# Kernel optimization log

Measured on AMD Instinct MI355X. Metric: run time of the kernel, lower is better.

The kernel has to match this reference:

```python
import jax, jax.numpy as jnp
import numpy as np

B, S, H = 32, 512, 768
VOCAB, MAX_POS, TYPE_VOCAB = 30522, 512, 2
N_COLS, MAX_HLEN = 32, 16
EPS = 1e-12


def setup_inputs() -> dict:
    key = jax.random.key(0)
    ks = jax.random.split(key, 16)
    input_ids = jax.random.randint(ks[0], (B, S), 0, VOCAB)
    header_ids = jax.random.randint(ks[1], (B, N_COLS, MAX_HLEN), 0, VOCAB)
    token_type_ids = jax.random.randint(ks[2], (B, S), 0, TYPE_VOCAB)
    match_type_ids = jax.random.randint(ks[3], (B, S), 0, 11)
    type_idx = jax.random.randint(ks[4], (B, S), 0, 6)
    # distinct scatter positions per batch row (the original dict keys ki are unique)
    col_pos = jnp.sort(jnp.argsort(jax.random.uniform(ks[5], (B, S)), axis=1)[:, :N_COLS], axis=1)
    col_idx = jax.random.randint(ks[6], (B, N_COLS), 0, N_COLS)
    header_len = jax.random.randint(ks[7], (B, N_COLS), 0, MAX_HLEN + 1)  # 0 -> skip
    word_emb = jax.random.normal(ks[8], (VOCAB, H), dtype=jnp.float32) * 0.02
    pos_emb = jax.random.normal(ks[9], (MAX_POS, H), dtype=jnp.float32) * 0.02
    tok_type_emb = jax.random.normal(ks[10], (TYPE_VOCAB, H), dtype=jnp.float32) * 0.02
    match_emb = jax.random.normal(ks[11], (11, H), dtype=jnp.float32) * 0.02
    type_emb = jax.random.normal(ks[12], (6, H), dtype=jnp.float32) * 0.02
    ln_w = jnp.ones((H,), dtype=jnp.float32)
    ln_b = jnp.zeros((H,), dtype=jnp.float32)
    return {"input_ids": input_ids, "header_ids": header_ids,
            "token_type_ids": token_type_ids, "match_type_ids": match_type_ids,
            "type_idx": type_idx, "col_pos": col_pos, "col_idx": col_idx,
            "header_len": header_len, "word_emb": word_emb, "pos_emb": pos_emb,
            "tok_type_emb": tok_type_emb, "match_emb": match_emb,
            "type_emb": type_emb, "ln_w": ln_w, "ln_b": ln_b}


def reference(input_ids, header_ids, token_type_ids, match_type_ids, type_idx,
              col_pos, col_idx, header_len, word_emb, pos_emb, tok_type_emb,
              match_emb, type_emb, ln_w, ln_b):
    b, s = input_ids.shape
    words = word_emb[input_ids]                    # [B,S,H]
    header = word_emb[header_ids]                  # [B,C,L,H]
    L = header_ids.shape[2]
    # variable-length mean pool over header tokens
    mask = (jnp.arange(L)[None, None, :] < header_len[:, :, None]).astype(words.dtype)
    denom = jnp.maximum(header_len, 1).astype(words.dtype)[..., None]
    pooled = jnp.einsum('bclh,bcl->bch', header, mask) / denom   # [B,C,H]
    # scatter pooled column embeddings into word embeddings at col_pos (skip len==0)
    b_idx = jnp.arange(b)[:, None]
    sel = pooled[b_idx, col_idx]                   # [B,C,H]
    valid = (header_len[b_idx, col_idx] > 0)[..., None]
    cur = words[b_idx, col_pos]
    words = words.at[b_idx, col_pos].set(jnp.where(valid, sel, cur))
    emb = (words
           + pos_emb[jnp.arange(s)][None, :, :]
           + tok_type_emb[token_type_ids]
           + match_emb[match_type_ids]
           + type_emb[type_idx])
    # TF-style LayerNorm (eps inside sqrt)
    u = emb.mean(-1, keepdims=True)
    var = jnp.square(emb - u).mean(-1, keepdims=True)
    x = (emb - u) / jnp.sqrt(var + EPS)
    return ln_w * x + ln_b
```

## Files before the change

### kernel.cpp

```cpp
#include <hip/hip_runtime.h>

#define B_ 32
#define S_ 512
#define H_ 768
#define C_ 32
#define L_ 16

__global__ __launch_bounds__(256) void bert_emb_kernel(
    const int* __restrict__ input_ids,
    const int* __restrict__ header_ids,
    const int* __restrict__ token_type_ids,
    const int* __restrict__ match_type_ids,
    const int* __restrict__ type_idx,
    const int* __restrict__ col_pos,
    const int* __restrict__ col_idx,
    const int* __restrict__ header_len,
    const float* __restrict__ word_emb,
    const float* __restrict__ pos_emb,
    const float* __restrict__ tok_type_emb,
    const float* __restrict__ match_emb,
    const float* __restrict__ type_emb,
    const float* __restrict__ ln_w,
    const float* __restrict__ ln_b,
    float* __restrict__ out)
{
    const int tok  = blockIdx.x * 4 + (threadIdx.x >> 6);
    const int lane = threadIdx.x & 63;
    const int b    = tok >> 9;
    const int s    = tok & (S_ - 1);

    const int cq = lane & 31;
    const int cp = col_pos[(b << 5) + cq];
    unsigned long long m = __ballot(cp == s) & 0xffffffffULL;
    int use_pool = 0, ci = 0, hlen = 0;
    if (m) {
        const int cm = __ffsll((unsigned long long)m) - 1;
        ci   = col_idx[(b << 5) + cm];
        hlen = header_len[(b << 5) + ci];
        use_pool = (hlen > 0);
    }

    const int h = lane << 2;
    float a0x, a0y, a0z, a0w, a1x, a1y, a1z, a1w, a2x, a2y, a2z, a2w;

    if (use_pool) {
        a0x=a0y=a0z=a0w=a1x=a1y=a1z=a1w=a2x=a2y=a2z=a2w=0.f;
        const int* hid = header_ids + ((b << 5) + ci) * L_;
        for (int l = 0; l < hlen; ++l) {
            const float* r = word_emb + (size_t)hid[l] * H_ + h;
            float4 v0 = *reinterpret_cast<const float4*>(r);
            float4 v1 = *reinterpret_cast<const float4*>(r + 256);
            float4 v2 = *reinterpret_cast<const float4*>(r + 512);
            a0x+=v0.x; a0y+=v0.y; a0z+=v0.z; a0w+=v0.w;
            a1x+=v1.x; a1y+=v1.y; a1z+=v1.z; a1w+=v1.w;
            a2x+=v2.x; a2y+=v2.y; a2z+=v2.z; a2w+=v2.w;
        }
        const float inv = 1.0f / (float)hlen;
        a0x*=inv; a0y*=inv; a0z*=inv; a0w*=inv;
        a1x*=inv; a1y*=inv; a1z*=inv; a1w*=inv;
        a2x*=inv; a2y*=inv; a2z*=inv; a2w*=inv;
    } else {
        const float* r = word_emb + (size_t)input_ids[tok] * H_ + h;
        float4 v0 = *reinterpret_cast<const float4*>(r);
        float4 v1 = *reinterpret_cast<const float4*>(r + 256);
        float4 v2 = *reinterpret_cast<const float4*>(r + 512);
        a0x=v0.x; a0y=v0.y; a0z=v0.z; a0w=v0.w;
        a1x=v1.x; a1y=v1.y; a1z=v1.z; a1w=v1.w;
        a2x=v2.x; a2y=v2.y; a2z=v2.z; a2w=v2.w;
    }

    {
        const float* r = pos_emb + s * H_ + h;
        float4 v0 = *reinterpret_cast<const float4*>(r);
        float4 v1 = *reinterpret_cast<const float4*>(r + 256);
        float4 v2 = *reinterpret_cast<const float4*>(r + 512);
        a0x+=v0.x; a0y+=v0.y; a0z+=v0.z; a0w+=v0.w;
        a1x+=v1.x; a1y+=v1.y; a1z+=v1.z; a1w+=v1.w;
        a2x+=v2.x; a2y+=v2.y; a2z+=v2.z; a2w+=v2.w;
    }
    {
        const float* r = tok_type_emb + token_type_ids[tok] * H_ + h;
        float4 v0 = *reinterpret_cast<const float4*>(r);
        float4 v1 = *reinterpret_cast<const float4*>(r + 256);
        float4 v2 = *reinterpret_cast<const float4*>(r + 512);
        a0x+=v0.x; a0y+=v0.y; a0z+=v0.z; a0w+=v0.w;
        a1x+=v1.x; a1y+=v1.y; a1z+=v1.z; a1w+=v1.w;
        a2x+=v2.x; a2y+=v2.y; a2z+=v2.z; a2w+=v2.w;
    }
    {
        const float* r = match_emb + match_type_ids[tok] * H_ + h;
        float4 v0 = *reinterpret_cast<const float4*>(r);
        float4 v1 = *reinterpret_cast<const float4*>(r + 256);
        float4 v2 = *reinterpret_cast<const float4*>(r + 512);
        a0x+=v0.x; a0y+=v0.y; a0z+=v0.z; a0w+=v0.w;
        a1x+=v1.x; a1y+=v1.y; a1z+=v1.z; a1w+=v1.w;
        a2x+=v2.x; a2y+=v2.y; a2z+=v2.z; a2w+=v2.w;
    }
    {
        const float* r = type_emb + type_idx[tok] * H_ + h;
        float4 v0 = *reinterpret_cast<const float4*>(r);
        float4 v1 = *reinterpret_cast<const float4*>(r + 256);
        float4 v2 = *reinterpret_cast<const float4*>(r + 512);
        a0x+=v0.x; a0y+=v0.y; a0z+=v0.z; a0w+=v0.w;
        a1x+=v1.x; a1y+=v1.y; a1z+=v1.z; a1w+=v1.w;
        a2x+=v2.x; a2y+=v2.y; a2z+=v2.z; a2w+=v2.w;
    }

    float s1 = a0x+a0y+a0z+a0w + a1x+a1y+a1z+a1w + a2x+a2y+a2z+a2w;
    float s2 = a0x*a0x+a0y*a0y+a0z*a0z+a0w*a0w
             + a1x*a1x+a1y*a1y+a1z*a1z+a1w*a1w
             + a2x*a2x+a2y*a2y+a2z*a2z+a2w*a2w;
    #pragma unroll
    for (int off = 32; off > 0; off >>= 1) {
        s1 += __shfl_xor(s1, off);
        s2 += __shfl_xor(s2, off);
    }
    const float mean = s1 * (1.0f / H_);
    float var = s2 * (1.0f / H_) - mean * mean;
    var = fmaxf(var, 0.0f);
    const float rstd = rsqrtf(var + 1e-12f);

    const float* wp = ln_w + h;
    const float* bp = ln_b + h;
    float* op = out + (size_t)tok * H_ + h;
    {
        float4 w = *reinterpret_cast<const float4*>(wp);
        float4 c = *reinterpret_cast<const float4*>(bp);
        float4 o;
        o.x=(a0x-mean)*rstd*w.x+c.x; o.y=(a0y-mean)*rstd*w.y+c.y;
        o.z=(a0z-mean)*rstd*w.z+c.z; o.w=(a0w-mean)*rstd*w.w+c.w;
        *reinterpret_cast<float4*>(op) = o;
    }
    {
        float4 w = *reinterpret_cast<const float4*>(wp + 256);
        float4 c = *reinterpret_cast<const float4*>(bp + 256);
        float4 o;
        o.x=(a1x-mean)*rstd*w.x+c.x; o.y=(a1y-mean)*rstd*w.y+c.y;
        o.z=(a1z-mean)*rstd*w.z+c.z; o.w=(a1w-mean)*rstd*w.w+c.w;
        *reinterpret_cast<float4*>(op + 256) = o;
    }
    {
        float4 w = *reinterpret_cast<const float4*>(wp + 512);
        float4 c = *reinterpret_cast<const float4*>(bp + 512);
        float4 o;
        o.x=(a2x-mean)*rstd*w.x+c.x; o.y=(a2y-mean)*rstd*w.y+c.y;
        o.z=(a2z-mean)*rstd*w.z+c.z; o.w=(a2w-mean)*rstd*w.w+c.w;
        *reinterpret_cast<float4*>(op + 512) = o;
    }
}

extern "C" void kernel_launch(void* const* d_in, const int* in_sizes, int n_in,
                              void* d_out, int out_size, void* d_ws, size_t ws_size,
                              hipStream_t stream) {
    const int* input_ids      = (const int*)d_in[0];
    const int* header_ids     = (const int*)d_in[1];
    const int* token_type_ids = (const int*)d_in[2];
    const int* match_type_ids = (const int*)d_in[3];
    const int* type_idx       = (const int*)d_in[4];
    const int* col_pos        = (const int*)d_in[5];
    const int* col_idx        = (const int*)d_in[6];
    const int* header_len     = (const int*)d_in[7];
    const float* word_emb     = (const float*)d_in[8];
    const float* pos_emb      = (const float*)d_in[9];
    const float* tok_type_emb = (const float*)d_in[10];
    const float* match_emb    = (const float*)d_in[11];
    const float* type_emb     = (const float*)d_in[12];
    const float* ln_w         = (const float*)d_in[13];
    const float* ln_b         = (const float*)d_in[14];
    float* out = (float*)d_out;

    bert_emb_kernel<<<(B_ * S_) / 4, 256, 0, stream>>>(
        input_ids, header_ids, token_type_ids, match_type_ids, type_idx,
        col_pos, col_idx, header_len, word_emb, pos_emb, tok_type_emb,
        match_emb, type_emb, ln_w, ln_b, out);
}
```

Baseline: 191.2 us.

## Precompute header mean-pooling in a separate kernel and use nontemporal output stores

A new pre-kernel computes the mean-pooled header embeddings for every column into workspace memory. The main kernel then reads one pooled row for scatter positions, so the variable-length gather loop no longer sits inside the per-token kernel and wave divergence goes away. Output writes now use nontemporal stores. The cost is an extra kernel launch, a workspace round trip, and pooling every column even when it is never selected.

```diff
diff --git a/kernel.cpp b/kernel.cpp
--- a/kernel.cpp
+++ b/kernel.cpp
@@ -5,10 +5,43 @@
 #define H_ 768
 #define C_ 32
 #define L_ 16
+#define VOCAB_ 30522
+
+typedef float f4 __attribute__((ext_vector_type(4)));
+
+__device__ __forceinline__ f4 ld4(const float* p) {
+    return *reinterpret_cast<const f4*>(p);
+}
+
+__global__ __launch_bounds__(256) void pool_kernel(
+    const int* __restrict__ header_ids,
+    const int* __restrict__ header_len,
+    const float* __restrict__ word_emb,
+    float* __restrict__ pooled)
+{
+    const int wi   = blockIdx.x * 4 + (threadIdx.x >> 6);
+    const int lane = threadIdx.x & 63;
+    const int hlen = header_len[wi];
+    if (hlen <= 0) return;
+
+    const int h = lane << 2;
+    const int* hid = header_ids + wi * L_;
+    f4 a0 = {0,0,0,0}, a1 = {0,0,0,0}, a2 = {0,0,0,0};
+    for (int l = 0; l < hlen; ++l) {
+        const float* r = word_emb + (size_t)hid[l] * H_ + h;
+        a0 += ld4(r);
+        a1 += ld4(r + 256);
+        a2 += ld4(r + 512);
+    }
+    const float inv = 1.0f / (float)hlen;
+    float* o = pooled + (size_t)wi * H_ + h;
+    *reinterpret_cast<f4*>(o)       = a0 * inv;
+    *reinterpret_cast<f4*>(o + 256) = a1 * inv;
+    *reinterpret_cast<f4*>(o + 512) = a2 * inv;
+}
 
 __global__ __launch_bounds__(256) void bert_emb_kernel(
     const int* __restrict__ input_ids,
-    const int* __restrict__ header_ids,
     const int* __restrict__ token_type_ids,
     const int* __restrict__ match_type_ids,
     const int* __restrict__ type_idx,
@@ -22,6 +55,7 @@
     const float* __restrict__ type_emb,
     const float* __restrict__ ln_w,
     const float* __restrict__ ln_b,
+    const float* __restrict__ pooled,
     float* __restrict__ out)
 {
     const int tok  = blockIdx.x * 4 + (threadIdx.x >> 6);
@@ -29,123 +63,69 @@
     const int b    = tok >> 9;
     const int s    = tok & (S_ - 1);
 
-    const int cq = lane & 31;
-    const int cp = col_pos[(b << 5) + cq];
+    const int cp = col_pos[(b << 5) + (lane & 31)];
     unsigned long long m = __ballot(cp == s) & 0xffffffffULL;
-    int use_pool = 0, ci = 0, hlen = 0;
+    const float* wrow;
     if (m) {
-        const int cm = __ffsll((unsigned long long)m) - 1;
-        ci   = col_idx[(b << 5) + cm];
-        hlen = header_len[(b << 5) + ci];
-        use_pool = (hlen > 0);
+        const int cm = __ffsll(m) - 1;
+        const int ci = col_idx[(b << 5) + cm];
+        if (header_len[(b << 5) + ci] > 0)
+            wrow = pooled + (size_t)((b << 5) + ci) * H_;
+        else
+            wrow = word_emb + (size_t)input_ids[tok] * H_;
+    } else {
+        wrow = word_emb + (size_t)input_ids[tok] * H_;
     }
 
     const int h = lane << 2;
-    float a0x, a0y, a0z, a0w, a1x, a1y, a1z, a1w, a2x, a2y, a2z, a2w;
-
-    if (use_pool) {
-        a0x=a0y=a0z=a0w=a1x=a1y=a1z=a1w=a2x=a2y=a2z=a2w=0.f;
-        const int* hid = header_ids + ((b << 5) + ci) * L_;
-        for (int l = 0; l < hlen; ++l) {
-            const float* r = word_emb + (size_t)hid[l] * H_ + h;
-            float4 v0 = *reinterpret_cast<const float4*>(r);
-            float4 v1 = *reinterpret_cast<const float4*>(r + 256);
-            float4 v2 = *reinterpret_cast<const float4*>(r + 512);
-            a0x+=v0.x; a0y+=v0.y; a0z+=v0.z; a0w+=v0.w;
-            a1x+=v1.x; a1y+=v1.y; a1z+=v1.z; a1w+=v1.w;
-            a2x+=v2.x; a2y+=v2.y; a2z+=v2.z; a2w+=v2.w;
-        }
-        const float inv = 1.0f / (float)hlen;
-        a0x*=inv; a0y*=inv; a0z*=inv; a0w*=inv;
-        a1x*=inv; a1y*=inv; a1z*=inv; a1w*=inv;
-        a2x*=inv; a2y*=inv; a2z*=inv; a2w*=inv;
-    } else {
-        const float* r = word_emb + (size_t)input_ids[tok] * H_ + h;
-        float4 v0 = *reinterpret_cast<const float4*>(r);
-        float4 v1 = *reinterpret_cast<const float4*>(r + 256);
-        float4 v2 = *reinterpret_cast<const float4*>(r + 512);
-        a0x=v0.x; a0y=v0.y; a0z=v0.z; a0w=v0.w;
-        a1x=v1.x; a1y=v1.y; a1z=v1.z; a1w=v1.w;
-        a2x=v2.x; a2y=v2.y; a2z=v2.z; a2w=v2.w;
-    }
-
+    f4 a0 = ld4(wrow + h);
+    f4 a1 = ld4(wrow + h + 256);
+    f4 a2 = ld4(wrow + h + 512);
     {
         const float* r = pos_emb + s * H_ + h;
-        float4 v0 = *reinterpret_cast<const float4*>(r);
-        float4 v1 = *reinterpret_cast<const float4*>(r + 256);
-        float4 v2 = *reinterpret_cast<const float4*>(r + 512);
-        a0x+=v0.x; a0y+=v0.y; a0z+=v0.z; a0w+=v0.w;
-        a1x+=v1.x; a1y+=v1.y; a1z+=v1.z; a1w+=v1.w;
-        a2x+=v2.x; a2y+=v2.y; a2z+=v2.z; a2w+=v2.w;
+        a0 += ld4(r); a1 += ld4(r + 256); a2 += ld4(r + 512);
     }
     {
         const float* r = tok_type_emb + token_type_ids[tok] * H_ + h;
-        float4 v0 = *reinterpret_cast<const float4*>(r);
-        float4 v1 = *reinterpret_cast<const float4*>(r + 256);
-        float4 v2 = *reinterpret_cast<const float4*>(r + 512);
-        a0x+=v0.x; a0y+=v0.y; a0z+=v0.z; a0w+=v0.w;
-        a1x+=v1.x; a1y+=v1.y; a1z+=v1.z; a1w+=v1.w;
-        a2x+=v2.x; a2y+=v2.y; a2z+=v2.z; a2w+=v2.w;
+        a0 += ld4(r); a1 += ld4(r + 256); a2 += ld4(r + 512);
     }
     {
         const float* r = match_emb + match_type_ids[tok] * H_ + h;
-        float4 v0 = *reinterpret_cast<const float4*>(r);
-        float4 v1 = *reinterpret_cast<const float4*>(r + 256);
-        float4 v2 = *reinterpret_cast<const float4*>(r + 512);
-        a0x+=v0.x; a0y+=v0.y; a0z+=v0.z; a0w+=v0.w;
-        a1x+=v1.x; a1y+=v1.y; a1z+=v1.z; a1w+=v1.w;
-        a2x+=v2.x; a2y+=v2.y; a2z+=v2.z; a2w+=v2.w;
+        a0 += ld4(r); a1 += ld4(r + 256); a2 += ld4(r + 512);
     }
     {
         const float* r = type_emb + type_idx[tok] * H_ + h;
-        float4 v0 = *reinterpret_cast<const float4*>(r);
-        float4 v1 = *reinterpret_cast<const float4*>(r + 256);
-        float4 v2 = *reinterpret_cast<const float4*>(r + 512);
-        a0x+=v0.x; a0y+=v0.y; a0z+=v0.z; a0w+=v0.w;
-        a1x+=v1.x; a1y+=v1.y; a1z+=v1.z; a1w+=v1.w;
-        a2x+=v2.x; a2y+=v2.y; a2z+=v2.z; a2w+=v2.w;
+        a0 += ld4(r); a1 += ld4(r + 256); a2 += ld4(r + 512);
     }
 
-    float s1 = a0x+a0y+a0z+a0w + a1x+a1y+a1z+a1w + a2x+a2y+a2z+a2w;
-    float s2 = a0x*a0x+a0y*a0y+a0z*a0z+a0w*a0w
-             + a1x*a1x+a1y*a1y+a1z*a1z+a1w*a1w
-             + a2x*a2x+a2y*a2y+a2z*a2z+a2w*a2w;
+    float s1 = a0.x+a0.y+a0.z+a0.w + a1.x+a1.y+a1.z+a1.w + a2.x+a2.y+a2.z+a2.w;
+    float s2 = a0.x*a0.x+a0.y*a0.y+a0.z*a0.z+a0.w*a0.w
+             + a1.x*a1.x+a1.y*a1.y+a1.z*a1.z+a1.w*a1.w
+             + a2.x*a2.x+a2.y*a2.y+a2.z*a2.z+a2.w*a2.w;
     #pragma unroll
     for (int off = 32; off > 0; off >>= 1) {
         s1 += __shfl_xor(s1, off);
         s2 += __shfl_xor(s2, off);
     }
     const float mean = s1 * (1.0f / H_);
-    float var = s2 * (1.0f / H_) - mean * mean;
-    var = fmaxf(var, 0.0f);
+    float var = fmaxf(s2 * (1.0f / H_) - mean * mean, 0.0f);
     const float rstd = rsqrtf(var + 1e-12f);
 
-    const float* wp = ln_w + h;
-    const float* bp = ln_b + h;
     float* op = out + (size_t)tok * H_ + h;
     {
-        float4 w = *reinterpret_cast<const float4*>(wp);
-        float4 c = *reinterpret_cast<const float4*>(bp);
-        float4 o;
-        o.x=(a0x-mean)*rstd*w.x+c.x; o.y=(a0y-mean)*rstd*w.y+c.y;
-        o.z=(a0z-mean)*rstd*w.z+c.z; o.w=(a0w-mean)*rstd*w.w+c.w;
-        *reinterpret_cast<float4*>(op) = o;
+        f4 w = ld4(ln_w + h), c = ld4(ln_b + h);
+        f4 o = (a0 - mean) * rstd * w + c;
+        __builtin_nontemporal_store(o, reinterpret_cast<f4*>(op));
     }
     {
-        float4 w = *reinterpret_cast<const float4*>(wp + 256);
-        float4 c = *reinterpret_cast<const float4*>(bp + 256);
-        float4 o;
-        o.x=(a1x-mean)*rstd*w.x+c.x; o.y=(a1y-mean)*rstd*w.y+c.y;
-        o.z=(a1z-mean)*rstd*w.z+c.z; o.w=(a1w-mean)*rstd*w.w+c.w;
-        *reinterpret_cast<float4*>(op + 256) = o;
+        f4 w = ld4(ln_w + h + 256), c = ld4(ln_b + h + 256);
+        f4 o = (a1 - mean) * rstd * w + c;
+        __builtin_nontemporal_store(o, reinterpret_cast<f4*>(op + 256));
     }
     {
-        float4 w = *reinterpret_cast<const float4*>(wp + 512);
-        float4 c = *reinterpret_cast<const float4*>(bp + 512);
-        float4 o;
-        o.x=(a2x-mean)*rstd*w.x+c.x; o.y=(a2y-mean)*rstd*w.y+c.y;
-        o.z=(a2z-mean)*rstd*w.z+c.z; o.w=(a2w-mean)*rstd*w.w+c.w;
-        *reinterpret_cast<float4*>(op + 512) = o;
+        f4 w = ld4(ln_w + h + 512), c = ld4(ln_b + h + 512);
+        f4 o = (a2 - mean) * rstd * w + c;
+        __builtin_nontemporal_store(o, reinterpret_cast<f4*>(op + 512));
     }
 }
 
@@ -167,10 +147,14 @@
     const float* type_emb     = (const float*)d_in[12];
     const float* ln_w         = (const float*)d_in[13];
     const float* ln_b         = (const float*)d_in[14];
-    float* out = (float*)d_out;
+    float* out    = (float*)d_out;
+    float* pooled = (float*)d_ws;
+
+    pool_kernel<<<(B_ * C_) / 4, 256, 0, stream>>>(
+        header_ids, header_len, word_emb, pooled);
 
     bert_emb_kernel<<<(B_ * S_) / 4, 256, 0, stream>>>(
-        input_ids, header_ids, token_type_ids, match_type_ids, type_idx,
+        input_ids, token_type_ids, match_type_ids, type_idx,
         col_pos, col_idx, header_len, word_emb, pos_emb, tok_type_emb,
-        match_emb, type_emb, ln_w, ln_b, out);
+        match_emb, type_emb, ln_w, ln_b, pooled, out);
 }
```

Result: slower. 203.1 us (+6.2%).
